# Optimization experiments

Measured on AMD Instinct MI355X. Metric: run time of the kernel, lower is better.

## Reference

```python
import jax, jax.numpy as jnp
import numpy as np

B, S, D = 32, 2048, 64

def setup_inputs() -> dict:
    key = jax.random.key(0)
    kq, kk, kv = jax.random.split(key, 3)
    queries = jax.random.normal(kq, (B, S, D), dtype=jnp.float32)
    keys = jax.random.normal(kk, (B, S, D), dtype=jnp.float32)
    values = jax.random.normal(kv, (B, S, D), dtype=jnp.float32)
    return {"queries": queries, "keys": keys, "values": values}

def reference(queries, keys, values):
    d = queries.shape[-1]
    scale = 1.0 / jnp.sqrt(jnp.asarray(d, queries.dtype))
    # scores: [B, Sq, Sk]
    scores = jnp.einsum('bqd,bkd->bqk', queries, keys) * scale
    attn = jax.nn.softmax(scores, axis=-1)
    # dropout prob is 0 in init_kwargs -> identity at eval/train
    return jnp.einsum('bqk,bkd->bqd', attn, values)
```

## Files before the change

kernel.cpp:

```cpp
#include <hip/hip_runtime.h>

typedef short    s16x8 __attribute__((ext_vector_type(8)));
typedef float    f32x4 __attribute__((ext_vector_type(4)));
typedef unsigned u32x4 __attribute__((ext_vector_type(4)));
typedef unsigned short ushort_t;

#define BB 32
#define SS 2048
#define DD 64
#define QBLK 64
#define KVBLK 64
#define NQB (SS / QBLK)
#define NTILES (SS / KVBLK)

#define QSCALE (0.125f * 1.44269504088896340736f)

#define V_OFF 8192
#define BUFSZ 16384

union U8 { u32x4 u; s16x8 s; };

__device__ __forceinline__ unsigned pk2bf(float lo, float hi) {
  unsigned r;
  asm("v_cvt_pk_bf16_f32 %0, %1, %2" : "=v"(r) : "v"(lo), "v"(hi));
  return r;
}

__device__ __forceinline__ void gll16(const void* g, void* l) {
  __builtin_amdgcn_global_load_lds(
      (const __attribute__((address_space(1))) void*)g,
      (__attribute__((address_space(3))) void*)l, 16, 0, 0);
}

#define BARRIER() asm volatile("s_waitcnt vmcnt(0) lgkmcnt(0)\ns_barrier" ::: "memory")

__global__ __launch_bounds__(256, 8)
void prep(const float* __restrict__ K, const float* __restrict__ V,
          ushort_t* __restrict__ Kb, ushort_t* __restrict__ Vt) {
  __shared__ ushort_t tl[64 * 66];
  const int bid = blockIdx.x, tid = threadIdx.x;
  if (bid < 2048) {
    const size_t base = (size_t)bid * 2048 + tid * 8;
    const float4 x = *(const float4*)(K + base);
    const float4 y = *(const float4*)(K + base + 4);
    u32x4 v = (u32x4){ pk2bf(x.x * QSCALE, x.y * QSCALE), pk2bf(x.z * QSCALE, x.w * QSCALE),
                       pk2bf(y.x * QSCALE, y.y * QSCALE), pk2bf(y.z * QSCALE, y.w * QSCALE) };
    *(u32x4*)(Kb + base) = v;
  } else {
    const int b2 = bid - 2048;
    const int b = b2 >> 5, t = b2 & 31;
    const int r = tid >> 2, dq = tid & 3;
    const int kp = ((r >> 5) * 4 + ((r >> 2) & 3)) * 8 + ((r >> 4) & 1) * 4 + (r & 3);
    const float* src = V + ((size_t)b * SS + t * KVBLK + r) * DD + dq * 16;
    float f[16];
    *(float4*)(f + 0)  = *(const float4*)(src + 0);
    *(float4*)(f + 4)  = *(const float4*)(src + 4);
    *(float4*)(f + 8)  = *(const float4*)(src + 8);
    *(float4*)(f + 12) = *(const float4*)(src + 12);
#pragma unroll
    for (int j = 0; j < 16; ++j) {
      union { float fv; unsigned u; } cv; cv.fv = f[j];
      tl[(dq * 16 + j) * 66 + kp] = (ushort_t)((cv.u + 0x7FFF + ((cv.u >> 16) & 1)) >> 16);
    }
    __syncthreads();
    const int d = tid >> 2, ch = tid & 3;
    ushort_t* dst = Vt + ((size_t)b * DD + d) * SS + t * KVBLK + ch * 16;
#pragma unroll
    for (int h = 0; h < 2; ++h) {
      const unsigned* ls = (const unsigned*)(tl + d * 66 + ch * 16 + h * 8);
      u32x4 o = (u32x4){ ls[0], ls[1], ls[2], ls[3] };
      *(u32x4*)(dst + h * 8) = o;
    }
  }
}

__global__ __launch_bounds__(256, 4)
void attn_fwd(const float* __restrict__ Q, const ushort_t* __restrict__ Kb,
              const ushort_t* __restrict__ Vt, float* __restrict__ O) {
  __shared__ __align__(16) char smem[2 * BUFSZ];
  const int tid  = threadIdx.x;
  const int w    = tid >> 6;
  const int lane = tid & 63;
  const int l15  = lane & 15;
  const int l16  = lane >> 4;

  const int bid0  = blockIdx.x;
  const int wid   = (bid0 & 7) * 128 + (bid0 >> 3);
  const int batch = wid >> 5;
  const int qb    = wid & 31;
  const size_t bstride = (size_t)batch * SS * DD;
  const int qrow0 = qb * QBLK + w * 16;

  s16x8 aq[2];
#pragma unroll
  for (int dh = 0; dh < 2; ++dh) {
    const float* qp = Q + bstride + (size_t)(qrow0 + l15) * DD + dh * 32 + l16 * 8;
    const float4 x = *(const float4*)qp;
    const float4 y = *(const float4*)(qp + 4);
    U8 u;
    u.u = (u32x4){ pk2bf(x.x, x.y), pk2bf(x.z, x.w), pk2bf(y.x, y.y), pk2bf(y.z, y.w) };
    aq[dh] = u.s;
  }

  f32x4 oT[4];
#pragma unroll
  for (int dt = 0; dt < 4; ++dt) oT[dt] = (f32x4){0.f, 0.f, 0.f, 0.f};
  float mrun = -1e30f;
  float lsum = 0.f;

  const int s0  = w * 128 + lane;
  const int r0  = s0 >> 3;
  const int lc0 = (s0 & 7) ^ (r0 & 7);
  const ushort_t* gk0 = Kb + bstride + (size_t)r0 * DD + lc0 * 8;
  const ushort_t* gk1 = gk0 + 8 * DD;
  const ushort_t* gv0 = Vt + (size_t)batch * DD * SS + (size_t)r0 * SS + lc0 * 8;
  const ushort_t* gv1 = gv0 + 8 * SS;
  char* lK = smem + w * 2048;
  char* lV = smem + V_OFF + w * 2048;

  auto ISSUE = [&](int t, int boff) {
    const size_t ko = (size_t)t * (KVBLK * DD);
    const size_t vo = (size_t)t * KVBLK;
    gll16(gk0 + ko, lK + boff);
    gll16(gk1 + ko, lK + boff + 1024);
    gll16(gv0 + vo, lV + boff);
    gll16(gv1 + vo, lV + boff + 1024);
  };

  auto compute = [&](int off) {
    s16x8 bk[4][2];
#pragma unroll
    for (int kc = 0; kc < 4; ++kc)
#pragma unroll
      for (int dh = 0; dh < 2; ++dh)
        bk[kc][dh] = *(const s16x8*)(smem + off + (kc * 16 + l15) * 128 +
                                     (((dh * 4 + l16) ^ (l15 & 7)) << 4));
    f32x4 s[4];
    __builtin_amdgcn_s_setprio(1);
#pragma unroll
    for (int kc = 0; kc < 4; ++kc) {
      s[kc] = (f32x4){0.f, 0.f, 0.f, 0.f};
      s[kc] = __builtin_amdgcn_mfma_f32_16x16x32_bf16(bk[kc][0], aq[0], s[kc], 0, 0, 0);
      s[kc] = __builtin_amdgcn_mfma_f32_16x16x32_bf16(bk[kc][1], aq[1], s[kc], 0, 0, 0);
    }
    __builtin_amdgcn_s_setprio(0);

    float m01 = fmaxf(fmaxf(fmaxf(s[0][0], s[0][1]), fmaxf(s[0][2], s[0][3])),
                      fmaxf(fmaxf(s[1][0], s[1][1]), fmaxf(s[1][2], s[1][3])));
    float m23 = fmaxf(fmaxf(fmaxf(s[2][0], s[2][1]), fmaxf(s[2][2], s[2][3])),
                      fmaxf(fmaxf(s[3][0], s[3][1]), fmaxf(s[3][2], s[3][3])));
    float mx = fmaxf(m01, m23);
    mx = fmaxf(mx, __shfl_xor(mx, 16));
    mx = fmaxf(mx, __shfl_xor(mx, 32));
    const int skip = __all(mx <= mrun + 8.0f);
    if (!skip) {
      const float mnew = fmaxf(mrun, mx);
      const float scl  = __builtin_amdgcn_exp2f(mrun - mnew);
      lsum *= scl;
#pragma unroll
      for (int dt = 0; dt < 4; ++dt) oT[dt] = oT[dt] * scl;
      mrun = mnew;
    }
    s16x8 vt[4][2];
#pragma unroll
    for (int dt = 0; dt < 4; ++dt)
#pragma unroll
      for (int kc2 = 0; kc2 < 2; ++kc2)
        vt[dt][kc2] = *(const s16x8*)(smem + off + V_OFF + (dt * 16 + l15) * 128 +
                                      (((kc2 * 4 + l16) ^ (l15 & 7)) << 4));
    float p[4][4];
#pragma unroll
    for (int kc = 0; kc < 4; ++kc)
#pragma unroll
      for (int r = 0; r < 4; ++r)
        p[kc][r] = __builtin_amdgcn_exp2f(s[kc][r] - mrun);
    lsum += ((((p[0][0] + p[0][1]) + (p[0][2] + p[0][3])) +
              ((p[1][0] + p[1][1]) + (p[1][2] + p[1][3]))) +
             (((p[2][0] + p[2][1]) + (p[2][2] + p[2][3])) +
              ((p[3][0] + p[3][1]) + (p[3][2] + p[3][3]))));
    U8 pb0, pb1;
    pb0.u = (u32x4){ pk2bf(p[0][0], p[0][1]), pk2bf(p[0][2], p[0][3]),
                     pk2bf(p[1][0], p[1][1]), pk2bf(p[1][2], p[1][3]) };
    pb1.u = (u32x4){ pk2bf(p[2][0], p[2][1]), pk2bf(p[2][2], p[2][3]),
                     pk2bf(p[3][0], p[3][1]), pk2bf(p[3][2], p[3][3]) };
    __builtin_amdgcn_s_setprio(1);
#pragma unroll
    for (int dt = 0; dt < 4; ++dt) {
      oT[dt] = __builtin_amdgcn_mfma_f32_16x16x32_bf16(vt[dt][0], pb0.s, oT[dt], 0, 0, 0);
      oT[dt] = __builtin_amdgcn_mfma_f32_16x16x32_bf16(vt[dt][1], pb1.s, oT[dt], 0, 0, 0);
    }
    __builtin_amdgcn_s_setprio(0);
  };

  ISSUE(0, 0);
  asm volatile("s_waitcnt vmcnt(0)" ::: "memory");
  __builtin_amdgcn_s_barrier();
  for (int i = 0; i < NTILES / 2 - 1; ++i) {
    ISSUE(2 * i + 1, BUFSZ); compute(0);     BARRIER();
    ISSUE(2 * i + 2, 0);     compute(BUFSZ); BARRIER();
  }
  ISSUE(NTILES - 1, BUFSZ);
  compute(0);
  BARRIER();
  compute(BUFSZ);

  float lr = lsum;
  lr += __shfl_xor(lr, 16);
  lr += __shfl_xor(lr, 32);
  const float inv = 1.0f / lr;
  float* ob = O + bstride + (size_t)(qrow0 + l15) * DD + l16 * 4;
#pragma unroll
  for (int dt = 0; dt < 4; ++dt)
#pragma unroll
    for (int r = 0; r < 4; ++r)
      ob[dt * 16 + r] = oT[dt][r] * inv;
}

extern "C" void kernel_launch(void* const* d_in, const int* in_sizes, int n_in,
                              void* d_out, int out_size, void* d_ws, size_t ws_size,
                              hipStream_t stream) {
  const float* Q = (const float*)d_in[0];
  const float* K = (const float*)d_in[1];
  const float* V = (const float*)d_in[2];
  float* Oo = (float*)d_out;

  const size_t elems = (size_t)BB * SS * DD;
  const size_t need  = 2 * elems * sizeof(ushort_t);
  if (ws_size < need) return;
  ushort_t* Kb = (ushort_t*)d_ws;
  ushort_t* Vt = Kb + elems;

  hipLaunchKernelGGL(prep, dim3(3072), dim3(256), 0, stream, K, V, Kb, Vt);
  hipLaunchKernelGGL(attn_fwd, dim3(BB * NQB), dim3(256), 0, stream, Q, Kb, Vt, Oo);
}
```

Before: 65.50 us.

## Software-pipeline QK of next tile with softmax and PV of current tile

```diff
diff --git a/kernel.cpp b/kernel.cpp
--- a/kernel.cpp
+++ b/kernel.cpp
@@ -15,8 +15,11 @@
 
 #define QSCALE (0.125f * 1.44269504088896340736f)
 
-#define V_OFF 8192
-#define BUFSZ 16384
+#define KB0 0
+#define KB1 8192
+#define VB0 16384
+#define VB1 24576
+#define VB2 32768
 
 union U8 { u32x4 u; s16x8 s; };
 
@@ -33,6 +36,7 @@
 }
 
 #define BARRIER() asm volatile("s_waitcnt vmcnt(0) lgkmcnt(0)\ns_barrier" ::: "memory")
+#define LBAR()    asm volatile("s_waitcnt lgkmcnt(0)\ns_barrier" ::: "memory")
 
 __global__ __launch_bounds__(256, 8)
 void prep(const float* __restrict__ K, const float* __restrict__ V,
@@ -77,7 +81,7 @@
 __global__ __launch_bounds__(256, 4)
 void attn_fwd(const float* __restrict__ Q, const ushort_t* __restrict__ Kb,
               const ushort_t* __restrict__ Vt, float* __restrict__ O) {
-  __shared__ __align__(16) char smem[2 * BUFSZ];
+  __shared__ __align__(16) char smem[40960];
   const int tid  = threadIdx.x;
   const int w    = tid >> 6;
   const int lane = tid & 63;
@@ -115,27 +119,25 @@
   const ushort_t* gk1 = gk0 + 8 * DD;
   const ushort_t* gv0 = Vt + (size_t)batch * DD * SS + (size_t)r0 * SS + lc0 * 8;
   const ushort_t* gv1 = gv0 + 8 * SS;
-  char* lK = smem + w * 2048;
-  char* lV = smem + V_OFF + w * 2048;
-
-  auto ISSUE = [&](int t, int boff) {
+  char* lB = smem + w * 2048;
+
+  auto ISSUE = [&](int t, int koff, int voff) {
     const size_t ko = (size_t)t * (KVBLK * DD);
     const size_t vo = (size_t)t * KVBLK;
-    gll16(gk0 + ko, lK + boff);
-    gll16(gk1 + ko, lK + boff + 1024);
-    gll16(gv0 + vo, lV + boff);
-    gll16(gv1 + vo, lV + boff + 1024);
+    gll16(gk0 + ko, lB + koff);
+    gll16(gk1 + ko, lB + koff + 1024);
+    gll16(gv0 + vo, lB + voff);
+    gll16(gv1 + vo, lB + voff + 1024);
   };
 
-  auto compute = [&](int off) {
+  auto QK = [&](int koff, f32x4 (&s)[4]) {
     s16x8 bk[4][2];
 #pragma unroll
     for (int kc = 0; kc < 4; ++kc)
 #pragma unroll
       for (int dh = 0; dh < 2; ++dh)
-        bk[kc][dh] = *(const s16x8*)(smem + off + (kc * 16 + l15) * 128 +
+        bk[kc][dh] = *(const s16x8*)(smem + koff + (kc * 16 + l15) * 128 +
                                      (((dh * 4 + l16) ^ (l15 & 7)) << 4));
-    f32x4 s[4];
     __builtin_amdgcn_s_setprio(1);
 #pragma unroll
     for (int kc = 0; kc < 4; ++kc) {
@@ -144,7 +146,9 @@
       s[kc] = __builtin_amdgcn_mfma_f32_16x16x32_bf16(bk[kc][1], aq[1], s[kc], 0, 0, 0);
     }
     __builtin_amdgcn_s_setprio(0);
-
+  };
+
+  auto SMPV = [&](int voff, f32x4 (&s)[4]) {
     float m01 = fmaxf(fmaxf(fmaxf(s[0][0], s[0][1]), fmaxf(s[0][2], s[0][3])),
                       fmaxf(fmaxf(s[1][0], s[1][1]), fmaxf(s[1][2], s[1][3])));
     float m23 = fmaxf(fmaxf(fmaxf(s[2][0], s[2][1]), fmaxf(s[2][2], s[2][3])),
@@ -166,7 +170,7 @@
     for (int dt = 0; dt < 4; ++dt)
 #pragma unroll
       for (int kc2 = 0; kc2 < 2; ++kc2)
-        vt[dt][kc2] = *(const s16x8*)(smem + off + V_OFF + (dt * 16 + l15) * 128 +
+        vt[dt][kc2] = *(const s16x8*)(smem + voff + (dt * 16 + l15) * 128 +
                                       (((kc2 * 4 + l16) ^ (l15 & 7)) << 4));
     float p[4][4];
 #pragma unroll
@@ -192,17 +196,25 @@
     __builtin_amdgcn_s_setprio(0);
   };
 
-  ISSUE(0, 0);
+  f32x4 SA[4], SB[4];
+
+  ISSUE(0, KB0, VB0);
+  ISSUE(1, KB1, VB1);
   asm volatile("s_waitcnt vmcnt(0)" ::: "memory");
   __builtin_amdgcn_s_barrier();
-  for (int i = 0; i < NTILES / 2 - 1; ++i) {
-    ISSUE(2 * i + 1, BUFSZ); compute(0);     BARRIER();
-    ISSUE(2 * i + 2, 0);     compute(BUFSZ); BARRIER();
+  QK(KB0, SA);
+  LBAR();
+
+  for (int i = 0; i < 5; ++i) {
+    ISSUE(6*i + 2, KB0, VB2); QK(KB1, SB); SMPV(VB0, SA); BARRIER();
+    ISSUE(6*i + 3, KB1, VB0); QK(KB0, SA); SMPV(VB1, SB); BARRIER();
+    ISSUE(6*i + 4, KB0, VB1); QK(KB1, SB); SMPV(VB2, SA); BARRIER();
+    ISSUE(6*i + 5, KB1, VB2); QK(KB0, SA); SMPV(VB0, SB); BARRIER();
+    ISSUE(6*i + 6, KB0, VB0); QK(KB1, SB); SMPV(VB1, SA); BARRIER();
+    ISSUE(6*i + 7, KB1, VB1); QK(KB0, SA); SMPV(VB2, SB); BARRIER();
   }
-  ISSUE(NTILES - 1, BUFSZ);
-  compute(0);
-  BARRIER();
-  compute(BUFSZ);
+  QK(KB1, SB); SMPV(VB0, SA); BARRIER();
+  SMPV(VB1, SB);
 
   float lr = lsum;
   lr += __shfl_xor(lr, 16);
```

Result: no change. 65.52 us (+0.0%).
